# Optimization experiments

Measured on AMD Instinct MI355X. Metric: run time of the kernel, lower is better.

## Reference

```python
import jax, jax.numpy as jnp
import numpy as np

B, F, R, O = 32768, 64, 64, 64  # batch, in_features, rules, out_features


def setup_inputs() -> dict:
    key = jax.random.key(0)
    k1, k2, k3, k4, k5 = jax.random.split(key, 5)
    X = jax.random.normal(k1, (B, F), dtype=jnp.float32)
    tt = jax.random.normal(k2, (1, F, R), dtype=jnp.float32) * 0.01
    mean = jax.random.normal(k3, (1, F, R), dtype=jnp.float32)
    # std is a learned positive scale (set by _rule_initialization); keep it away from 0
    std = jax.random.uniform(k4, (1, F, R), dtype=jnp.float32, minval=0.5, maxval=1.5)
    W = jax.random.normal(k5, (O, R * (F + 1)), dtype=jnp.float32) * 0.02  # nn.Linear weight [out, in]
    return {"X": X, "tt": tt, "mean": mean, "std": std, "W": W}


def reference(X, tt, mean, std, W):
    t = jnp.tanh(tt)                                  # [1,F,R]
    z = (X[:, :, None] - mean) / std                  # [B,F,R]
    g = jnp.exp(-(z * z))                             # Gaussian membership [B,F,R]
    m = g * t + 0.5 * (1.0 - t)                       # affine blend toward 0.5
    fire = jnp.prod(m, axis=1)                        # product t-norm over features -> [B,R]
    w = fire / jnp.sum(fire, axis=1, keepdims=True)   # normalize over rules
    ones = jnp.ones((X.shape[0], 1), dtype=X.dtype)
    Xa = jnp.concatenate([X, ones], axis=1)           # [B,F+1]
    feat = (Xa[:, :, None] * w[:, None, :]).reshape(X.shape[0], -1)  # [B,(F+1)*R], row-major (f outer, r inner)
    return feat @ W.T                                 # [B,O]
```

## Files before the change

kernel.cpp:

```cpp
#include <hip/hip_runtime.h>
#include <hip/hip_bf16.h>

#define F 64
#define R 64
#define O 64
#define BLOCK_B 32

typedef short bf16x8 __attribute__((ext_vector_type(8)));
typedef float f32x4 __attribute__((ext_vector_type(4)));

static __device__ __forceinline__ short f2bf(float f) {
    unsigned u = __builtin_bit_cast(unsigned, f);
    unsigned r = (u + 0x7fffu + ((u >> 16) & 1u)) >> 16;
    return (short)r;
}

__global__ __launch_bounds__(256) void fq_prep(
        const float* __restrict__ tt, const float* __restrict__ mean,
        const float* __restrict__ std_, const float* __restrict__ W,
        float* __restrict__ prm, unsigned short* __restrict__ Wpk)
{
    const int tg = blockIdx.x * 256 + threadIdx.x;
    if (tg < 65 * 512) {
        const int f    = tg >> 9;
        const int u8   = tg & 511;
        const int lane = u8 & 63;
        const int kk   = (u8 >> 6) & 1;
        const int nt   = u8 >> 7;
        const int o    = nt * 16 + (lane & 15);
        const int rb   = ((lane >> 4) << 3) + kk * 32;
        const float* src = W + o * 4160 + f * 64 + rb;
        unsigned short v[8];
#pragma unroll
        for (int j = 0; j < 8; ++j) v[j] = (unsigned short)f2bf(src[j]);
        *(bf16x8*)(Wpk + (size_t)tg * 8) = *(bf16x8*)v;
    } else if (tg < 65 * 512 + 4096) {
        const int u = tg - 65 * 512;
        float sd = std_[u];
        float mn = mean[u];
        float th = tanhf(tt[u]);
        float s  = 1.2011224087864498f / sd;
        float4 p;
        p.x = s;
        p.y = mn * s;
        p.z = th;
        p.w = 0.5f * (1.0f - th);
        ((float4*)prm)[u] = p;
    }
}

__global__ __launch_bounds__(512, 8) void fq_main(
        const float* __restrict__ X,
        const float4* __restrict__ prm,
        const bf16x8* __restrict__ Wp,
        float* __restrict__ out)
{
    __shared__ float xt[64][BLOCK_B];
    __shared__ float fire_lds[BLOCK_B][R + 1];
    __shared__ float rinv[BLOCK_B];

    const int t    = threadIdx.x;
    const int lane = t & 63;
    const int w    = __builtin_amdgcn_readfirstlane(t >> 6);
    const int b0   = blockIdx.x * BLOCK_B;

    {
        const int row = t >> 4;
        const int f4  = (t & 15) * 4;
        float4 xv = *(const float4*)(X + (size_t)(b0 + row) * 64 + f4);
        xt[f4 + 0][row] = xv.x;
        xt[f4 + 1][row] = xv.y;
        xt[f4 + 2][row] = xv.z;
        xt[f4 + 3][row] = xv.w;
    }

    float fire[4] = {1.f, 1.f, 1.f, 1.f};
    for (int f = 0; f < F; ++f) {
        float4 p = prm[f * 64 + lane];
#pragma unroll
        for (int i = 0; i < 4; ++i) {
            float x = X[(size_t)(b0 + 4 * w + i) * 64 + f];
            float z = __builtin_fmaf(x, p.x, -p.y);
            float g = __builtin_amdgcn_exp2f(-(z * z));
            fire[i] *= __builtin_fmaf(g, p.z, p.w);
        }
    }
#pragma unroll
    for (int i = 0; i < 4; ++i)
        fire_lds[4 * w + i][lane] = fire[i];
    __syncthreads();

    if (t < BLOCK_B) {
        float s = 0.0f;
#pragma unroll 8
        for (int r = 0; r < 64; ++r) s += fire_lds[t][r];
        rinv[t] = 1.0f / s;
    }
    __syncthreads();

    const int m_in  = lane & 15;
    const int quad  = lane >> 4;
    const int mrow  = w & 1;
    const int nt    = w >> 1;
    const int myrow = 16 * mrow + m_in;
    const float rs  = rinv[myrow];

    bf16x8 wfrag[2];
#pragma unroll
    for (int kk = 0; kk < 2; ++kk)
#pragma unroll
        for (int j = 0; j < 8; ++j)
            wfrag[kk][j] = f2bf(fire_lds[myrow][quad * 8 + j + kk * 32] * rs);

    f32x4 acc = (f32x4){0.f, 0.f, 0.f, 0.f};
    const f32x4 z4 = (f32x4){0.f, 0.f, 0.f, 0.f};
    const int xoff = 16 * mrow + quad * 4;

    for (int f = 0; f < F; ++f) {
        bf16x8 bf0 = Wp[f * 512 + nt * 128 + lane];
        bf16x8 bf1 = Wp[f * 512 + nt * 128 + 64 + lane];
        f32x4 U = __builtin_amdgcn_mfma_f32_16x16x32_bf16(wfrag[0], bf0, z4, 0, 0, 0);
        U = __builtin_amdgcn_mfma_f32_16x16x32_bf16(wfrag[1], bf1, U, 0, 0, 0);
        f32x4 xv = *(const f32x4*)(&xt[f][xoff]);
#pragma unroll
        for (int reg = 0; reg < 4; ++reg)
            acc[reg] = __builtin_fmaf(xv[reg], U[reg], acc[reg]);
    }

    {
        bf16x8 bf0 = Wp[64 * 512 + nt * 128 + lane];
        bf16x8 bf1 = Wp[64 * 512 + nt * 128 + 64 + lane];
        f32x4 U = __builtin_amdgcn_mfma_f32_16x16x32_bf16(wfrag[0], bf0, z4, 0, 0, 0);
        U = __builtin_amdgcn_mfma_f32_16x16x32_bf16(wfrag[1], bf1, U, 0, 0, 0);
#pragma unroll
        for (int reg = 0; reg < 4; ++reg)
            acc[reg] += U[reg];
    }

#pragma unroll
    for (int reg = 0; reg < 4; ++reg) {
        int row = b0 + 16 * mrow + quad * 4 + reg;
        out[(size_t)row * 64 + nt * 16 + m_in] = acc[reg];
    }
}

extern "C" void kernel_launch(void* const* d_in, const int* in_sizes, int n_in,
                              void* d_out, int out_size, void* d_ws, size_t ws_size,
                              hipStream_t stream) {
    const float* X    = (const float*)d_in[0];
    const float* tt   = (const float*)d_in[1];
    const float* mean = (const float*)d_in[2];
    const float* std_ = (const float*)d_in[3];
    const float* W    = (const float*)d_in[4];
    float* out = (float*)d_out;

    float* prm = (float*)d_ws;
    unsigned short* Wpk = (unsigned short*)((char*)d_ws + 65536);

    fq_prep<<<146, 256, 0, stream>>>(tt, mean, std_, W, prm, Wpk);

    const int nblocks = 32768 / BLOCK_B;
    fq_main<<<nblocks, 512, 0, stream>>>(X, (const float4*)prm,
                                         (const bf16x8*)Wpk, out);
}
```

Measured before the change: 114.5 us.

## Fold x scaling into MFMA A-fragments and process 64 rows per block

Doubles the batch tile to 64 rows so each wave computes two 16-row MFMA tiles that share the same W fragment loads. Instead of running fresh MFMAs per feature and applying x with VALU FMAs afterwards, each normalized rule-weight fragment is pre-scaled by x[b,f] and accumulated directly in the MFMA accumulator. The packed W layout is reordered so each n-tile reads contiguously. The fire computation uses packed f32x2 math, and the row-sum normalization is spread across all threads using shuffles. In exchange it adds per-feature VALU work to build bf16 fragments, uses truncating bf16 conversion, and halves the occupancy hint in launch bounds.

```diff
diff --git a/kernel.cpp b/kernel.cpp
--- a/kernel.cpp
+++ b/kernel.cpp
@@ -4,15 +4,31 @@
 #define F 64
 #define R 64
 #define O 64
-#define BLOCK_B 32
+#define BLOCK_B 64
 
 typedef short bf16x8 __attribute__((ext_vector_type(8)));
 typedef float f32x4 __attribute__((ext_vector_type(4)));
+typedef float f32x2 __attribute__((ext_vector_type(2)));
 
 static __device__ __forceinline__ short f2bf(float f) {
     unsigned u = __builtin_bit_cast(unsigned, f);
     unsigned r = (u + 0x7fffu + ((u >> 16) & 1u)) >> 16;
     return (short)r;
+}
+
+static __device__ __forceinline__ unsigned pack2bf_trunc(float lo, float hi) {
+    return __builtin_amdgcn_perm(__builtin_bit_cast(unsigned, hi),
+                                 __builtin_bit_cast(unsigned, lo), 0x07060302u);
+}
+
+static __device__ __forceinline__ bf16x8 mk_frag(const f32x2* wn, float x) {
+    union { bf16x8 v; unsigned u[4]; } r;
+#pragma unroll
+    for (int i = 0; i < 4; ++i) {
+        f32x2 p = wn[i] * x;
+        r.u[i] = pack2bf_trunc(p.x, p.y);
+    }
+    return r.v;
 }
 
 __global__ __launch_bounds__(256) void fq_prep(
@@ -33,7 +49,8 @@
         unsigned short v[8];
 #pragma unroll
         for (int j = 0; j < 8; ++j) v[j] = (unsigned short)f2bf(src[j]);
-        *(bf16x8*)(Wpk + (size_t)tg * 8) = *(bf16x8*)v;
+        const int dst = ((nt * 65 + f) * 2 + kk) * 64 + lane;
+        *(bf16x8*)(Wpk + (size_t)dst * 8) = *(bf16x8*)v;
     } else if (tg < 65 * 512 + 4096) {
         const int u = tg - 65 * 512;
         float sd = std_[u];
@@ -49,14 +66,13 @@
     }
 }
 
-__global__ __launch_bounds__(512, 8) void fq_main(
+__global__ __launch_bounds__(512, 4) void fq_main(
         const float* __restrict__ X,
         const float4* __restrict__ prm,
         const bf16x8* __restrict__ Wp,
         float* __restrict__ out)
 {
-    __shared__ float xt[64][BLOCK_B];
-    __shared__ float fire_lds[BLOCK_B][R + 1];
+    __shared__ __align__(16) float fire_lds[BLOCK_B][R + 4];
     __shared__ float rinv[BLOCK_B];
 
     const int t    = threadIdx.x;
@@ -64,83 +80,121 @@
     const int w    = __builtin_amdgcn_readfirstlane(t >> 6);
     const int b0   = blockIdx.x * BLOCK_B;
 
-    {
-        const int row = t >> 4;
-        const int f4  = (t & 15) * 4;
-        float4 xv = *(const float4*)(X + (size_t)(b0 + row) * 64 + f4);
-        xt[f4 + 0][row] = xv.x;
-        xt[f4 + 1][row] = xv.y;
-        xt[f4 + 2][row] = xv.z;
-        xt[f4 + 3][row] = xv.w;
-    }
-
-    float fire[4] = {1.f, 1.f, 1.f, 1.f};
+    f32x2 fire2[4];
+#pragma unroll
+    for (int i = 0; i < 4; ++i) fire2[i] = (f32x2){1.f, 1.f};
+
+    const float* Xb = X + (size_t)(b0 + 8 * w) * 64;
     for (int f = 0; f < F; ++f) {
         float4 p = prm[f * 64 + lane];
+        f32x2 t2 = (f32x2){p.z, p.z};
+        f32x2 c2 = (f32x2){p.w, p.w};
 #pragma unroll
         for (int i = 0; i < 4; ++i) {
-            float x = X[(size_t)(b0 + 4 * w + i) * 64 + f];
-            float z = __builtin_fmaf(x, p.x, -p.y);
-            float g = __builtin_amdgcn_exp2f(-(z * z));
-            fire[i] *= __builtin_fmaf(g, p.z, p.w);
+            float x0 = Xb[(2 * i) * 64 + f];
+            float x1 = Xb[(2 * i + 1) * 64 + f];
+            f32x2 z;
+            z.x = __builtin_fmaf(x0, p.x, -p.y);
+            z.y = __builtin_fmaf(x1, p.x, -p.y);
+            f32x2 nz = -(z * z);
+            f32x2 g;
+            g.x = __builtin_amdgcn_exp2f(nz.x);
+            g.y = __builtin_amdgcn_exp2f(nz.y);
+            fire2[i] *= g * t2 + c2;
         }
     }
 #pragma unroll
-    for (int i = 0; i < 4; ++i)
-        fire_lds[4 * w + i][lane] = fire[i];
+    for (int i = 0; i < 4; ++i) {
+        fire_lds[8 * w + 2 * i][lane]     = fire2[i].x;
+        fire_lds[8 * w + 2 * i + 1][lane] = fire2[i].y;
+    }
     __syncthreads();
 
-    if (t < BLOCK_B) {
-        float s = 0.0f;
-#pragma unroll 8
-        for (int r = 0; r < 64; ++r) s += fire_lds[t][r];
-        rinv[t] = 1.0f / s;
+    {
+        const int row = t >> 3;
+        const int c8  = (t & 7) * 8;
+        f32x4 s0 = *(const f32x4*)&fire_lds[row][c8];
+        f32x4 s1 = *(const f32x4*)&fire_lds[row][c8 + 4];
+        float s = (s0[0] + s0[1]) + (s0[2] + s0[3]) +
+                  (s1[0] + s1[1]) + (s1[2] + s1[3]);
+        s += __shfl_xor(s, 1);
+        s += __shfl_xor(s, 2);
+        s += __shfl_xor(s, 4);
+        if ((t & 7) == 0) rinv[row] = 1.0f / s;
     }
     __syncthreads();
 
-    const int m_in  = lane & 15;
-    const int quad  = lane >> 4;
-    const int mrow  = w & 1;
-    const int nt    = w >> 1;
-    const int myrow = 16 * mrow + m_in;
-    const float rs  = rinv[myrow];
-
-    bf16x8 wfrag[2];
-#pragma unroll
-    for (int kk = 0; kk < 2; ++kk)
-#pragma unroll
-        for (int j = 0; j < 8; ++j)
-            wfrag[kk][j] = f2bf(fire_lds[myrow][quad * 8 + j + kk * 32] * rs);
-
-    f32x4 acc = (f32x4){0.f, 0.f, 0.f, 0.f};
-    const f32x4 z4 = (f32x4){0.f, 0.f, 0.f, 0.f};
-    const int xoff = 16 * mrow + quad * 4;
-
-    for (int f = 0; f < F; ++f) {
-        bf16x8 bf0 = Wp[f * 512 + nt * 128 + lane];
-        bf16x8 bf1 = Wp[f * 512 + nt * 128 + 64 + lane];
-        f32x4 U = __builtin_amdgcn_mfma_f32_16x16x32_bf16(wfrag[0], bf0, z4, 0, 0, 0);
-        U = __builtin_amdgcn_mfma_f32_16x16x32_bf16(wfrag[1], bf1, U, 0, 0, 0);
-        f32x4 xv = *(const f32x4*)(&xt[f][xoff]);
-#pragma unroll
-        for (int reg = 0; reg < 4; ++reg)
-            acc[reg] = __builtin_fmaf(xv[reg], U[reg], acc[reg]);
+    const int m_in = lane & 15;
+    const int quad = lane >> 4;
+    const int nt   = w >> 1;
+    const int g    = w & 1;
+    const int ra   = 32 * g + m_in;
+    const int rb   = ra + 16;
+    const float rs_a = rinv[ra];
+    const float rs_b = rinv[rb];
+    const int q8 = quad * 8;
+
+    f32x2 wna[8], wnb[8];
+#pragma unroll
+    for (int kk = 0; kk < 2; ++kk) {
+        f32x4 a0 = *(const f32x4*)&fire_lds[ra][q8 + 32 * kk];
+        f32x4 a1 = *(const f32x4*)&fire_lds[ra][q8 + 32 * kk + 4];
+        f32x4 b0 = *(const f32x4*)&fire_lds[rb][q8 + 32 * kk];
+        f32x4 b1 = *(const f32x4*)&fire_lds[rb][q8 + 32 * kk + 4];
+        wna[kk * 4 + 0] = (f32x2){a0[0], a0[1]} * rs_a;
+        wna[kk * 4 + 1] = (f32x2){a0[2], a0[3]} * rs_a;
+        wna[kk * 4 + 2] = (f32x2){a1[0], a1[1]} * rs_a;
+        wna[kk * 4 + 3] = (f32x2){a1[2], a1[3]} * rs_a;
+        wnb[kk * 4 + 0] = (f32x2){b0[0], b0[1]} * rs_b;
+        wnb[kk * 4 + 1] = (f32x2){b0[2], b0[3]} * rs_b;
+        wnb[kk * 4 + 2] = (f32x2){b1[0], b1[1]} * rs_b;
+        wnb[kk * 4 + 3] = (f32x2){b1[2], b1[3]} * rs_b;
+    }
+
+    const bf16x8* wpb = Wp + (size_t)(nt * 130) * 64 + lane;
+    const float* Xa_p = X + (size_t)(b0 + ra) * 64;
+    const float* Xb_p = X + (size_t)(b0 + rb) * 64;
+
+    f32x4 acc_a = (f32x4){0.f, 0.f, 0.f, 0.f};
+    f32x4 acc_b = (f32x4){0.f, 0.f, 0.f, 0.f};
+
+    for (int f4 = 0; f4 < 16; ++f4) {
+        f32x4 xa4 = *(const f32x4*)(Xa_p + 4 * f4);
+        f32x4 xb4 = *(const f32x4*)(Xb_p + 4 * f4);
+#pragma unroll
+        for (int j = 0; j < 4; ++j) {
+            const int f = f4 * 4 + j;
+            bf16x8 bb0 = wpb[(2 * f) * 64];
+            bf16x8 bb1 = wpb[(2 * f + 1) * 64];
+            bf16x8 fa0 = mk_frag(wna + 0, xa4[j]);
+            bf16x8 fa1 = mk_frag(wna + 4, xa4[j]);
+            bf16x8 fb0 = mk_frag(wnb + 0, xb4[j]);
+            bf16x8 fb1 = mk_frag(wnb + 4, xb4[j]);
+            acc_a = __builtin_amdgcn_mfma_f32_16x16x32_bf16(fa0, bb0, acc_a, 0, 0, 0);
+            acc_a = __builtin_amdgcn_mfma_f32_16x16x32_bf16(fa1, bb1, acc_a, 0, 0, 0);
+            acc_b = __builtin_amdgcn_mfma_f32_16x16x32_bf16(fb0, bb0, acc_b, 0, 0, 0);
+            acc_b = __builtin_amdgcn_mfma_f32_16x16x32_bf16(fb1, bb1, acc_b, 0, 0, 0);
+        }
     }
 
     {
-        bf16x8 bf0 = Wp[64 * 512 + nt * 128 + lane];
-        bf16x8 bf1 = Wp[64 * 512 + nt * 128 + 64 + lane];
-        f32x4 U = __builtin_amdgcn_mfma_f32_16x16x32_bf16(wfrag[0], bf0, z4, 0, 0, 0);
-        U = __builtin_amdgcn_mfma_f32_16x16x32_bf16(wfrag[1], bf1, U, 0, 0, 0);
-#pragma unroll
-        for (int reg = 0; reg < 4; ++reg)
-            acc[reg] += U[reg];
+        bf16x8 bb0 = wpb[128 * 64];
+        bf16x8 bb1 = wpb[129 * 64];
+        bf16x8 fa0 = mk_frag(wna + 0, 1.0f);
+        bf16x8 fa1 = mk_frag(wna + 4, 1.0f);
+        bf16x8 fb0 = mk_frag(wnb + 0, 1.0f);
+        bf16x8 fb1 = mk_frag(wnb + 4, 1.0f);
+        acc_a = __builtin_amdgcn_mfma_f32_16x16x32_bf16(fa0, bb0, acc_a, 0, 0, 0);
+        acc_a = __builtin_amdgcn_mfma_f32_16x16x32_bf16(fa1, bb1, acc_a, 0, 0, 0);
+        acc_b = __builtin_amdgcn_mfma_f32_16x16x32_bf16(fb0, bb0, acc_b, 0, 0, 0);
+        acc_b = __builtin_amdgcn_mfma_f32_16x16x32_bf16(fb1, bb1, acc_b, 0, 0, 0);
     }
 
 #pragma unroll
     for (int reg = 0; reg < 4; ++reg) {
-        int row = b0 + 16 * mrow + quad * 4 + reg;
-        out[(size_t)row * 64 + nt * 16 + m_in] = acc[reg];
+        const int col = nt * 16 + m_in;
+        out[(size_t)(b0 + 32 * g + quad * 4 + reg) * 64 + col]      = acc_a[reg];
+        out[(size_t)(b0 + 32 * g + 16 + quad * 4 + reg) * 64 + col] = acc_b[reg];
     }
 }
 
```

Result: slower. 120.0 us (+4.8%).
